# Optimization experiments

Measured on AMD Instinct MI355X. Metric: run time of the kernel, lower is better.

Reference implementation:

```python
import jax, jax.numpy as jnp
import numpy as np

EMBED_DIM = 1024
NUM_HEADS = 16
HEAD_DIM = EMBED_DIM // NUM_HEADS
SCALE = HEAD_DIM ** -0.5


def setup_inputs() -> dict:
    key = jax.random.key(0)
    ks = jax.random.split(key, 5)
    B, N, C = 4, 2048, EMBED_DIM
    s = C ** -0.5
    return {
        "x": jax.random.normal(ks[0], (B, N, C), dtype=jnp.float32),
        "w_qkv": jax.random.normal(ks[1], (C, 3 * C), dtype=jnp.float32) * s,
        "b_qkv": jnp.zeros((3 * C,), dtype=jnp.float32),
        "w_proj": jax.random.normal(ks[2], (C, C), dtype=jnp.float32) * s,
        "b_proj": jnp.zeros((C,), dtype=jnp.float32),
    }


def reference(x, w_qkv, b_qkv, w_proj, b_proj):
    B, N, C = x.shape
    H, D = NUM_HEADS, HEAD_DIM
    qkv = x @ w_qkv + b_qkv                      # (B, N, 3C)
    qkv = qkv.reshape(B, N, 3, H, D)
    qkv = jnp.transpose(qkv, (2, 0, 3, 1, 4))    # (3, B, H, N, D)
    q, k, v = qkv[0], qkv[1], qkv[2]
    attn = jnp.einsum('bhnd,bhmd->bhnm', q, k) * SCALE
    attn = jax.nn.softmax(attn, axis=-1)
    out = jnp.einsum('bhnm,bhmd->bhnd', attn, v)  # (B, H, N, D)
    out = jnp.transpose(out, (0, 2, 1, 3)).reshape(B, N, C)
    return out @ w_proj + b_proj
```

## Files before the change

kernel.cpp:

```cpp
#include <hip/hip_runtime.h>

typedef __attribute__((ext_vector_type(8))) short short8v;
typedef __attribute__((ext_vector_type(4))) short short4v;
typedef __attribute__((ext_vector_type(4))) float float4v;
typedef __attribute__((ext_vector_type(4))) unsigned short ushort4v;
typedef __attribute__((ext_vector_type(8))) unsigned short ushort8v;

#define GLOBAL_AS __attribute__((address_space(1)))
#define LDS_AS __attribute__((address_space(3)))

__device__ __forceinline__ void async_cp16(const void* g, void* l) {
  __builtin_amdgcn_global_load_lds((const GLOBAL_AS void*)g, (LDS_AS void*)l, 16, 0, 0);
}

__device__ __forceinline__ unsigned short f2bf(float f) {
  unsigned u = __float_as_uint(f);
  u += 0x7fffu + ((u >> 16) & 1u);
  return (unsigned short)(u >> 16);
}

#if defined(__HIP_DEVICE_COMPILE__)
#if __has_builtin(__builtin_amdgcn_exp2f)
#define EXP2F(x) __builtin_amdgcn_exp2f(x)
#else
#define EXP2F(x) exp2f(x)
#endif
#else
#define EXP2F(x) exp2f(x)
#endif

#if defined(__HIP_DEVICE_COMPILE__) && __has_builtin(__builtin_amdgcn_cvt_pk_bf16_f32)
typedef __attribute__((ext_vector_type(2))) __bf16 bf16x2v;
__device__ __forceinline__ unsigned pk_bf16(float a, float b) {
  bf16x2v r = __builtin_amdgcn_cvt_pk_bf16_f32(a, b);
  return __builtin_bit_cast(unsigned, r);
}
#else
__device__ __forceinline__ unsigned pk_bf16(float a, float b) {
  return (unsigned)f2bf(a) | ((unsigned)f2bf(b) << 16);
}
#endif

#define MFMA_QK(a, b, c) __builtin_amdgcn_mfma_f32_16x16x32_bf16(a, b, c, 0, 0, 0)

__device__ __forceinline__ void wg_barrier() {
  asm volatile("" ::: "memory");
  __builtin_amdgcn_s_barrier();
  asm volatile("" ::: "memory");
}


__global__ __launch_bounds__(256) void cvt_f32_bf16(const float* __restrict__ src,
                                                    unsigned short* __restrict__ dst) {
  int i = blockIdx.x * 256 + threadIdx.x;
  float4 v = ((const float4*)src)[i];
  ushort4v o;
  o.x = f2bf(v.x); o.y = f2bf(v.y); o.z = f2bf(v.z); o.w = f2bf(v.w);
  ((ushort4v*)dst)[i] = o;
}

__global__ __launch_bounds__(256) void transpose_w(const float* __restrict__ src,
                                                   unsigned short* __restrict__ dst,
                                                   int K, int N) {
  __shared__ float tile[64][65];
  int k0 = blockIdx.x * 64, n0 = blockIdx.y * 64;
  int t = threadIdx.x;
  int tc = t & 15, tr = t >> 4;
#pragma unroll
  for (int p = 0; p < 4; p++) {
    int r = tr + p * 16;
    float4 v = *(const float4*)(src + (size_t)(k0 + r) * N + n0 + tc * 4);
    tile[r][tc * 4 + 0] = v.x; tile[r][tc * 4 + 1] = v.y;
    tile[r][tc * 4 + 2] = v.z; tile[r][tc * 4 + 3] = v.w;
  }
  __syncthreads();
#pragma unroll
  for (int p = 0; p < 4; p++) {
    int rn = tr + p * 16;
    ushort4v o;
    o.x = f2bf(tile[tc * 4 + 0][rn]);
    o.y = f2bf(tile[tc * 4 + 1][rn]);
    o.z = f2bf(tile[tc * 4 + 2][rn]);
    o.w = f2bf(tile[tc * 4 + 3][rn]);
    *(ushort4v*)(dst + (size_t)(n0 + rn) * K + k0 + tc * 4) = o;
  }
}

__device__ __forceinline__ void stage128x32(const unsigned short* __restrict__ src,
                                            unsigned short* dst, int r0, int k0, int tid) {
#pragma unroll
  for (int p = 0; p < 2; p++) {
    int idx = p * 256 + tid;
    int row = idx >> 2, s = idx & 3;
    int ch = s ^ ((row >> 1) & 3);
    async_cp16(src + (size_t)(r0 + row) * 1024 + k0 + ch * 8, dst + idx * 8);
  }
}


#define TT_STRIDE 136

__global__ __launch_bounds__(256) void gemm_qkv(const unsigned short* __restrict__ A,
                                                const unsigned short* __restrict__ BT,
                                                const float* __restrict__ bias,
                                                unsigned short* __restrict__ Qo,
                                                unsigned short* __restrict__ Ko,
                                                unsigned short* __restrict__ VTo) {
  __shared__ unsigned short smem[24576];
  int tid = threadIdx.x;
  int lane = tid & 63, w = tid >> 6, g = lane >> 4, c = lane & 15;
  int m0 = blockIdx.x * 128, n0 = blockIdx.y * 128;
  int wm = (w & 1) * 64, wn = (w >> 1) * 64;
  float4v acc[4][4] = {};

  stage128x32(A, smem + 0 * 4096, m0, 0, tid);
  stage128x32(BT, smem + 12288 + 0 * 4096, n0, 0, tid);
  stage128x32(A, smem + 1 * 4096, m0, 32, tid);
  stage128x32(BT, smem + 12288 + 1 * 4096, n0, 32, tid);
  asm volatile("s_waitcnt vmcnt(4)" ::: "memory");
  wg_barrier();

  int cb = 0;
  for (int t = 0; t < 32; ++t) {
    int nb = cb + 2; if (nb >= 3) nb -= 3;
    const unsigned short* Ap = smem + cb * 4096;
    const unsigned short* Bp = smem + 12288 + cb * 4096;

    short8v af[4], bf[4];
#pragma unroll
    for (int i = 0; i < 4; i++) {
      int r = wm + i * 16 + c;
      af[i] = *(const short8v*)(Ap + r * 32 + (g ^ ((r >> 1) & 3)) * 8);
    }
#pragma unroll
    for (int j = 0; j < 4; j++) {
      int r = wn + j * 16 + c;
      bf[j] = *(const short8v*)(Bp + r * 32 + (g ^ ((r >> 1) & 3)) * 8);
    }

    if (t + 2 < 32) {
      stage128x32(A, smem + nb * 4096, m0, (t + 2) * 32, tid);
      stage128x32(BT, smem + 12288 + nb * 4096, n0, (t + 2) * 32, tid);
    }

    __builtin_amdgcn_s_setprio(1);
#pragma unroll
    for (int i = 0; i < 4; i++)
#pragma unroll
      for (int j = 0; j < 4; j++)
        acc[i][j] = MFMA_QK(af[i], bf[j], acc[i][j]);
    __builtin_amdgcn_s_setprio(0);

    if (t < 30) { asm volatile("s_waitcnt vmcnt(4)" ::: "memory"); }
    else        { asm volatile("s_waitcnt vmcnt(0)" ::: "memory"); }
    wg_barrier();
    cb = cb + 1 == 3 ? 0 : cb + 1;
  }

  int which = n0 >> 10;
  if (which != 2) {
#pragma unroll
    for (int j = 0; j < 4; j++) {
      int ng = n0 + wn + j * 16 + c;
      float bv = bias[ng];
      int h = (ng & 1023) >> 6, d = ng & 63;
#pragma unroll
      for (int i = 0; i < 4; i++) {
#pragma unroll
        for (int r = 0; r < 4; r++) {
          int mg = m0 + wm + i * 16 + g * 4 + r;
          int b = mg >> 11, n = mg & 2047;
          float v = acc[i][j][r] + bv;
          if (which == 0)
            Qo[((size_t)(b * 16 + h) * 2048 + n) * 64 + d] = f2bf(v * 0.18033688011112042f);
          else
            Ko[((size_t)(b * 16 + h) * 2048 + n) * 64 + d] = f2bf(v);
        }
      }
    }
  } else {
    __syncthreads();
#pragma unroll
    for (int j = 0; j < 4; j++) {
      int nl = wn + j * 16 + c;
      float bv = bias[n0 + nl];
#pragma unroll
      for (int i = 0; i < 4; i++) {
        int ml = wm + i * 16 + g * 4;
        unsigned p0 = pk_bf16(acc[i][j][0] + bv, acc[i][j][1] + bv);
        unsigned p1 = pk_bf16(acc[i][j][2] + bv, acc[i][j][3] + bv);
        *(unsigned*)(smem + nl * TT_STRIDE + ml) = p0;
        *(unsigned*)(smem + nl * TT_STRIDE + ml + 2) = p1;
      }
    }
    __syncthreads();
    int rr = lane >> 4, tc = lane & 15;
    int P = tc & 3, g32 = tc >> 2;
    int b = m0 >> 11, mloc = m0 & 2047;
    int h0 = (n0 & 1023) >> 6;
#pragma unroll
    for (int s = 0; s < 8; s++) {
      int row = w * 32 + s * 4 + rr;
      int h = h0 + (row >> 6), d = row & 63;
      const unsigned short* bp = smem + row * TT_STRIDE + g32 * 32 + P * 4;
      union { unsigned long long q[2]; ushort8v v; } u;
      u.q[0] = *(const unsigned long long*)(bp);
      u.q[1] = *(const unsigned long long*)(bp + 16);
      size_t gaddr = ((size_t)(b * 16 + h) * 64 + d) * 2048 + mloc + g32 * 32 + P * 8;
      *(ushort8v*)(VTo + gaddr) = u.v;
    }
  }
}


#define NTOK 2048
#define BK 64

__device__ __forceinline__ short8v exppack(float4v a, float4v b2) {
  a.x = EXP2F(a.x); a.y = EXP2F(a.y); a.z = EXP2F(a.z); a.w = EXP2F(a.w);
  b2.x = EXP2F(b2.x); b2.y = EXP2F(b2.y); b2.z = EXP2F(b2.z); b2.w = EXP2F(b2.w);
  union { unsigned u[4]; short8v s; } cv;
  cv.u[0] = pk_bf16(a.x, a.y);
  cv.u[1] = pk_bf16(a.z, a.w);
  cv.u[2] = pk_bf16(b2.x, b2.y);
  cv.u[3] = pk_bf16(b2.z, b2.w);
  return cv.s;
}

__global__ __launch_bounds__(256, 2) void attn_kernel(const unsigned short* __restrict__ Qg,
                                                      const unsigned short* __restrict__ Kg,
                                                      const unsigned short* __restrict__ VTg,
                                                      unsigned short* __restrict__ Og) {
  __shared__ unsigned short Ks[2][BK * 64];
  __shared__ unsigned short VTs[2][64 * BK];

  int tid = threadIdx.x;
  int lane = tid & 63, w = tid >> 6, g = lane >> 4, c = lane & 15;
  int id = blockIdx.x;
  int xcd = id & 7, within = id >> 3;
  int bh = xcd * 8 + (within >> 3);
  int q0 = (within & 7) * 256;

  const unsigned short* Qb = Qg + (size_t)bh * NTOK * 64;
  const unsigned short* Kb = Kg + (size_t)bh * NTOK * 64;
  const unsigned short* VTb = VTg + (size_t)bh * 64 * NTOK;

  short8v qf[4][2];
#pragma unroll
  for (int nt = 0; nt < 4; nt++)
#pragma unroll
    for (int kk = 0; kk < 2; kk++)
      qf[nt][kk] = *(const short8v*)(Qb + (size_t)(q0 + w * 64 + nt * 16 + c) * 64 +
                                     kk * 32 + g * 8);

  short8v ones8;
#pragma unroll
  for (int i = 0; i < 8; i++) ones8[i] = (short)0x3F80;

  float4v lacc[4] = {};
  float4v o[4][4] = {};

#pragma unroll
  for (int p = 0; p < 2; p++) {
    int idx = p * 256 + tid;
    int row = idx >> 3, ch = idx & 7;
    async_cp16(Kb + (size_t)row * 64 + ((ch ^ (row & 7)) * 8), &Ks[0][idx * 8]);
    async_cp16(VTb + (size_t)row * NTOK + ((ch ^ (row & 7)) * 8), &VTs[0][idx * 8]);
  }

  for (int it = 0; it < NTOK / BK; it++) {
    int pb = it & 1;
    __syncthreads();

    if (it + 1 < NTOK / BK) {
      int kt = (it + 1) * BK;
#pragma unroll
      for (int p = 0; p < 2; p++) {
        int idx = p * 256 + tid;
        int row = idx >> 3, ch = idx & 7;
        async_cp16(Kb + (size_t)(kt + row) * 64 + ((ch ^ (row & 7)) * 8),
                   &Ks[1 - pb][idx * 8]);
        async_cp16(VTb + (size_t)row * NTOK + kt + ((ch ^ (row & 7)) * 8),
                   &VTs[1 - pb][idx * 8]);
      }
    }

    const unsigned short* Kp = &Ks[pb][0];
    const unsigned short* Vp = &VTs[pb][0];

    float4v stA[2][4] = {};
    float4v stB[2][4] = {};

    __builtin_amdgcn_s_setprio(1);
#pragma unroll
    for (int mth = 0; mth < 2; mth++) {
      int row = mth * 16 + c;
      short8v kf[2];
#pragma unroll
      for (int kk = 0; kk < 2; kk++) {
        int ch = (kk * 4 + g) ^ (row & 7);
        kf[kk] = *(const short8v*)(Kp + row * 64 + ch * 8);
      }
#pragma unroll
      for (int nt = 0; nt < 4; nt++)
#pragma unroll
        for (int kk = 0; kk < 2; kk++)
          stA[mth][nt] = MFMA_QK(kf[kk], qf[nt][kk], stA[mth][nt]);
    }
#pragma unroll
    for (int mth = 0; mth < 2; mth++) {
      int row = (2 + mth) * 16 + c;
      short8v kf[2];
#pragma unroll
      for (int kk = 0; kk < 2; kk++) {
        int ch = (kk * 4 + g) ^ (row & 7);
        kf[kk] = *(const short8v*)(Kp + row * 64 + ch * 8);
      }
#pragma unroll
      for (int nt = 0; nt < 4; nt++)
#pragma unroll
        for (int kk = 0; kk < 2; kk++)
          stB[mth][nt] = MFMA_QK(kf[kk], qf[nt][kk], stB[mth][nt]);
    }
    __builtin_amdgcn_s_setprio(0);

    short8v pa8A[4];
#pragma unroll
    for (int nt = 0; nt < 4; nt++) pa8A[nt] = exppack(stA[0][nt], stA[1][nt]);

    __builtin_amdgcn_s_setprio(1);
#pragma unroll
    for (int nt_o = 0; nt_o < 4; nt_o++) {
      int d = nt_o * 16 + c;
      int s = g ^ (d & 7);
      short8v vb8 = *(const short8v*)(Vp + d * BK + s * 8);
#pragma unroll
      for (int mt = 0; mt < 4; mt++)
        o[mt][nt_o] = MFMA_QK(pa8A[mt], vb8, o[mt][nt_o]);
    }
#pragma unroll
    for (int mt = 0; mt < 4; mt++)
      lacc[mt] = MFMA_QK(pa8A[mt], ones8, lacc[mt]);
    __builtin_amdgcn_s_setprio(0);

    short8v pa8B[4];
#pragma unroll
    for (int nt = 0; nt < 4; nt++) pa8B[nt] = exppack(stB[0][nt], stB[1][nt]);

    __builtin_amdgcn_s_setprio(1);
#pragma unroll
    for (int nt_o = 0; nt_o < 4; nt_o++) {
      int d = nt_o * 16 + c;
      int s = (4 + g) ^ (d & 7);
      short8v vb8 = *(const short8v*)(Vp + d * BK + s * 8);
#pragma unroll
      for (int mt = 0; mt < 4; mt++)
        o[mt][nt_o] = MFMA_QK(pa8B[mt], vb8, o[mt][nt_o]);
    }
#pragma unroll
    for (int mt = 0; mt < 4; mt++)
      lacc[mt] = MFMA_QK(pa8B[mt], ones8, lacc[mt]);
    __builtin_amdgcn_s_setprio(0);
  }

  int b = bh >> 4, h = bh & 15;
#pragma unroll
  for (int mt = 0; mt < 4; mt++) {
    float4v li;
#pragma unroll
    for (int r = 0; r < 4; r++) li[r] = 1.0f / lacc[mt][r];
#pragma unroll
    for (int nt_o = 0; nt_o < 4; nt_o++) {
      float4v v = o[mt][nt_o] * li;
      int col = h * 64 + nt_o * 16 + c;
      int rowbase = b * NTOK + q0 + w * 64 + mt * 16 + g * 4;
#pragma unroll
      for (int r = 0; r < 4; r++)
        Og[(size_t)(rowbase + r) * 1024 + col] = f2bf(v[r]);
    }
  }
}

__global__ __launch_bounds__(256) void gemm_proj(const unsigned short* __restrict__ A,
                                                 const unsigned short* __restrict__ BT,
                                                 const float* __restrict__ bias,
                                                 float* __restrict__ out) {
  __shared__ unsigned short smem[24576];
  int tid = threadIdx.x;
  int lane = tid & 63, w = tid >> 6, g = lane >> 4, c = lane & 15;
  int m0 = blockIdx.x * 128, n0 = blockIdx.y * 128;
  int wm = (w & 1) * 64, wn = (w >> 1) * 64;
  float4v acc[4][4] = {};

  stage128x32(A, smem + 0 * 4096, m0, 0, tid);
  stage128x32(BT, smem + 12288 + 0 * 4096, n0, 0, tid);
  stage128x32(A, smem + 1 * 4096, m0, 32, tid);
  stage128x32(BT, smem + 12288 + 1 * 4096, n0, 32, tid);
  asm volatile("s_waitcnt vmcnt(4)" ::: "memory");
  wg_barrier();

  int cb = 0;
  for (int t = 0; t < 32; ++t) {
    int nb = cb + 2; if (nb >= 3) nb -= 3;
    const unsigned short* Ap = smem + cb * 4096;
    const unsigned short* Bp = smem + 12288 + cb * 4096;

    short8v af[4], bf[4];
#pragma unroll
    for (int i = 0; i < 4; i++) {
      int r = wm + i * 16 + c;
      af[i] = *(const short8v*)(Ap + r * 32 + (g ^ ((r >> 1) & 3)) * 8);
    }
#pragma unroll
    for (int j = 0; j < 4; j++) {
      int r = wn + j * 16 + c;
      bf[j] = *(const short8v*)(Bp + r * 32 + (g ^ ((r >> 1) & 3)) * 8);
    }

    if (t + 2 < 32) {
      stage128x32(A, smem + nb * 4096, m0, (t + 2) * 32, tid);
      stage128x32(BT, smem + 12288 + nb * 4096, n0, (t + 2) * 32, tid);
    }

    __builtin_amdgcn_s_setprio(1);
#pragma unroll
    for (int i = 0; i < 4; i++)
#pragma unroll
      for (int j = 0; j < 4; j++)
        acc[i][j] = MFMA_QK(af[i], bf[j], acc[i][j]);
    __builtin_amdgcn_s_setprio(0);

    if (t < 30) { asm volatile("s_waitcnt vmcnt(4)" ::: "memory"); }
    else        { asm volatile("s_waitcnt vmcnt(0)" ::: "memory"); }
    wg_barrier();
    cb = cb + 1 == 3 ? 0 : cb + 1;
  }

#pragma unroll
  for (int j = 0; j < 4; j++) {
    int ng = n0 + wn + j * 16 + c;
    float bv = bias[ng];
#pragma unroll
    for (int i = 0; i < 4; i++) {
#pragma unroll
      for (int r = 0; r < 4; r++) {
        int mg = m0 + wm + i * 16 + g * 4 + r;
        out[(size_t)mg * 1024 + ng] = acc[i][j][r] + bv;
      }
    }
  }
}


extern "C" void kernel_launch(void* const* d_in, const int* in_sizes, int n_in,
                              void* d_out, int out_size, void* d_ws, size_t ws_size,
                              hipStream_t stream) {
  (void)in_sizes; (void)n_in; (void)out_size; (void)ws_size;
  const float* x = (const float*)d_in[0];
  const float* w_qkv = (const float*)d_in[1];
  const float* b_qkv = (const float*)d_in[2];
  const float* w_proj = (const float*)d_in[3];
  const float* b_proj = (const float*)d_in[4];
  float* out = (float*)d_out;

  unsigned short* x_bf = (unsigned short*)d_ws;
  unsigned short* wqkvT = x_bf + (size_t)8192 * 1024;
  unsigned short* wprojT = wqkvT + (size_t)3072 * 1024;
  unsigned short* qws = wprojT + (size_t)1024 * 1024;
  unsigned short* kws = qws + (size_t)8388608;
  unsigned short* vtws = kws + (size_t)8388608;
  unsigned short* aws = vtws + (size_t)8388608;

  cvt_f32_bf16<<<8192, 256, 0, stream>>>(x, x_bf);
  transpose_w<<<dim3(16, 48), 256, 0, stream>>>(w_qkv, wqkvT, 1024, 3072);
  transpose_w<<<dim3(16, 16), 256, 0, stream>>>(w_proj, wprojT, 1024, 1024);
  gemm_qkv<<<dim3(64, 24), 256, 0, stream>>>(x_bf, wqkvT, b_qkv, qws, kws, vtws);
  attn_kernel<<<512, 256, 0, stream>>>(qws, kws, vtws, aws);
  gemm_proj<<<dim3(64, 8), 256, 0, stream>>>(aws, wprojT, b_proj, out);
}
```

Measured before the change: 265.9 us.

## Halve attention query tile and load V directly from global

The attention kernel now processes 128 queries per block (32 per wave) instead of 256, doubling the grid to 1024 blocks and raising launch bounds to 4 blocks per CU. The V^T tile is no longer staged in LDS through async copies. Each lane reads its V fragments straight from global memory, which halves LDS use and cuts the registers needed for accumulators. The aim is higher occupancy and better latency hiding. In exchange, K tiles are reused across fewer queries, K/V traffic rises, and direct global V loads may stall the MFMA chain.

```diff
diff --git a/kernel.cpp b/kernel.cpp
--- a/kernel.cpp
+++ b/kernel.cpp
@@ -227,45 +227,45 @@
   return cv.s;
 }
 
-__global__ __launch_bounds__(256, 2) void attn_kernel(const unsigned short* __restrict__ Qg,
+__global__ __launch_bounds__(256, 4) void attn_kernel(const unsigned short* __restrict__ Qg,
                                                       const unsigned short* __restrict__ Kg,
                                                       const unsigned short* __restrict__ VTg,
                                                       unsigned short* __restrict__ Og) {
   __shared__ unsigned short Ks[2][BK * 64];
-  __shared__ unsigned short VTs[2][64 * BK];
 
   int tid = threadIdx.x;
   int lane = tid & 63, w = tid >> 6, g = lane >> 4, c = lane & 15;
   int id = blockIdx.x;
   int xcd = id & 7, within = id >> 3;
-  int bh = xcd * 8 + (within >> 3);
-  int q0 = (within & 7) * 256;
+  int bh = xcd * 8 + (within >> 4);
+  int q0 = (within & 15) * 128;
 
   const unsigned short* Qb = Qg + (size_t)bh * NTOK * 64;
   const unsigned short* Kb = Kg + (size_t)bh * NTOK * 64;
   const unsigned short* VTb = VTg + (size_t)bh * 64 * NTOK;
 
-  short8v qf[4][2];
-#pragma unroll
-  for (int nt = 0; nt < 4; nt++)
+  short8v qf[2][2];
+#pragma unroll
+  for (int nt = 0; nt < 2; nt++)
 #pragma unroll
     for (int kk = 0; kk < 2; kk++)
-      qf[nt][kk] = *(const short8v*)(Qb + (size_t)(q0 + w * 64 + nt * 16 + c) * 64 +
+      qf[nt][kk] = *(const short8v*)(Qb + (size_t)(q0 + w * 32 + nt * 16 + c) * 64 +
                                      kk * 32 + g * 8);
 
   short8v ones8;
 #pragma unroll
   for (int i = 0; i < 8; i++) ones8[i] = (short)0x3F80;
 
-  float4v lacc[4] = {};
-  float4v o[4][4] = {};
+  float4v lacc[2] = {};
+  float4v o[2][4] = {};
+
+  const unsigned short* vbase = VTb + (size_t)c * 2048 + g * 8;
 
 #pragma unroll
   for (int p = 0; p < 2; p++) {
     int idx = p * 256 + tid;
     int row = idx >> 3, ch = idx & 7;
     async_cp16(Kb + (size_t)row * 64 + ((ch ^ (row & 7)) * 8), &Ks[0][idx * 8]);
-    async_cp16(VTb + (size_t)row * NTOK + ((ch ^ (row & 7)) * 8), &VTs[0][idx * 8]);
   }
 
   for (int it = 0; it < NTOK / BK; it++) {
@@ -280,92 +280,58 @@
         int row = idx >> 3, ch = idx & 7;
         async_cp16(Kb + (size_t)(kt + row) * 64 + ((ch ^ (row & 7)) * 8),
                    &Ks[1 - pb][idx * 8]);
-        async_cp16(VTb + (size_t)row * NTOK + kt + ((ch ^ (row & 7)) * 8),
-                   &VTs[1 - pb][idx * 8]);
       }
     }
 
     const unsigned short* Kp = &Ks[pb][0];
-    const unsigned short* Vp = &VTs[pb][0];
-
-    float4v stA[2][4] = {};
-    float4v stB[2][4] = {};
-
-    __builtin_amdgcn_s_setprio(1);
-#pragma unroll
-    for (int mth = 0; mth < 2; mth++) {
-      int row = mth * 16 + c;
-      short8v kf[2];
-#pragma unroll
-      for (int kk = 0; kk < 2; kk++) {
-        int ch = (kk * 4 + g) ^ (row & 7);
-        kf[kk] = *(const short8v*)(Kp + row * 64 + ch * 8);
+
+#pragma unroll
+    for (int t = 0; t < 2; t++) {
+      int ch32 = it * 2 + t;
+      short8v vb[4];
+#pragma unroll
+      for (int nt_o = 0; nt_o < 4; nt_o++)
+        vb[nt_o] = *(const short8v*)(vbase + (size_t)nt_o * 32768 + ch32 * 32);
+
+      float4v st[2][2] = {};
+      __builtin_amdgcn_s_setprio(1);
+#pragma unroll
+      for (int mth = 0; mth < 2; mth++) {
+        int row = (t * 2 + mth) * 16 + c;
+        short8v kf[2];
+#pragma unroll
+        for (int kk = 0; kk < 2; kk++) {
+          int ch = (kk * 4 + g) ^ (row & 7);
+          kf[kk] = *(const short8v*)(Kp + row * 64 + ch * 8);
+        }
+#pragma unroll
+        for (int nt = 0; nt < 2; nt++)
+#pragma unroll
+          for (int kk = 0; kk < 2; kk++)
+            st[mth][nt] = MFMA_QK(kf[kk], qf[nt][kk], st[mth][nt]);
       }
-#pragma unroll
-      for (int nt = 0; nt < 4; nt++)
-#pragma unroll
-        for (int kk = 0; kk < 2; kk++)
-          stA[mth][nt] = MFMA_QK(kf[kk], qf[nt][kk], stA[mth][nt]);
-    }
-#pragma unroll
-    for (int mth = 0; mth < 2; mth++) {
-      int row = (2 + mth) * 16 + c;
-      short8v kf[2];
-#pragma unroll
-      for (int kk = 0; kk < 2; kk++) {
-        int ch = (kk * 4 + g) ^ (row & 7);
-        kf[kk] = *(const short8v*)(Kp + row * 64 + ch * 8);
-      }
-#pragma unroll
-      for (int nt = 0; nt < 4; nt++)
-#pragma unroll
-        for (int kk = 0; kk < 2; kk++)
-          stB[mth][nt] = MFMA_QK(kf[kk], qf[nt][kk], stB[mth][nt]);
-    }
-    __builtin_amdgcn_s_setprio(0);
-
-    short8v pa8A[4];
-#pragma unroll
-    for (int nt = 0; nt < 4; nt++) pa8A[nt] = exppack(stA[0][nt], stA[1][nt]);
-
-    __builtin_amdgcn_s_setprio(1);
-#pragma unroll
-    for (int nt_o = 0; nt_o < 4; nt_o++) {
-      int d = nt_o * 16 + c;
-      int s = g ^ (d & 7);
-      short8v vb8 = *(const short8v*)(Vp + d * BK + s * 8);
-#pragma unroll
-      for (int mt = 0; mt < 4; mt++)
-        o[mt][nt_o] = MFMA_QK(pa8A[mt], vb8, o[mt][nt_o]);
-    }
-#pragma unroll
-    for (int mt = 0; mt < 4; mt++)
-      lacc[mt] = MFMA_QK(pa8A[mt], ones8, lacc[mt]);
-    __builtin_amdgcn_s_setprio(0);
-
-    short8v pa8B[4];
-#pragma unroll
-    for (int nt = 0; nt < 4; nt++) pa8B[nt] = exppack(stB[0][nt], stB[1][nt]);
-
-    __builtin_amdgcn_s_setprio(1);
-#pragma unroll
-    for (int nt_o = 0; nt_o < 4; nt_o++) {
-      int d = nt_o * 16 + c;
-      int s = (4 + g) ^ (d & 7);
-      short8v vb8 = *(const short8v*)(Vp + d * BK + s * 8);
-#pragma unroll
-      for (int mt = 0; mt < 4; mt++)
-        o[mt][nt_o] = MFMA_QK(pa8B[mt], vb8, o[mt][nt_o]);
-    }
-#pragma unroll
-    for (int mt = 0; mt < 4; mt++)
-      lacc[mt] = MFMA_QK(pa8B[mt], ones8, lacc[mt]);
-    __builtin_amdgcn_s_setprio(0);
+      __builtin_amdgcn_s_setprio(0);
+
+      short8v pa8[2];
+#pragma unroll
+      for (int nt = 0; nt < 2; nt++) pa8[nt] = exppack(st[0][nt], st[1][nt]);
+
+      __builtin_amdgcn_s_setprio(1);
+#pragma unroll
+      for (int nt_o = 0; nt_o < 4; nt_o++)
+#pragma unroll
+        for (int mt = 0; mt < 2; mt++)
+          o[mt][nt_o] = MFMA_QK(pa8[mt], vb[nt_o], o[mt][nt_o]);
+#pragma unroll
+      for (int mt = 0; mt < 2; mt++)
+        lacc[mt] = MFMA_QK(pa8[mt], ones8, lacc[mt]);
+      __builtin_amdgcn_s_setprio(0);
+    }
   }
 
   int b = bh >> 4, h = bh & 15;
 #pragma unroll
-  for (int mt = 0; mt < 4; mt++) {
+  for (int mt = 0; mt < 2; mt++) {
     float4v li;
 #pragma unroll
     for (int r = 0; r < 4; r++) li[r] = 1.0f / lacc[mt][r];
@@ -373,7 +339,7 @@
     for (int nt_o = 0; nt_o < 4; nt_o++) {
       float4v v = o[mt][nt_o] * li;
       int col = h * 64 + nt_o * 16 + c;
-      int rowbase = b * NTOK + q0 + w * 64 + mt * 16 + g * 4;
+      int rowbase = b * NTOK + q0 + w * 32 + mt * 16 + g * 4;
 #pragma unroll
       for (int r = 0; r < 4; r++)
         Og[(size_t)(rowbase + r) * 1024 + col] = f2bf(v[r]);
@@ -475,6 +441,6 @@
   transpose_w<<<dim3(16, 48), 256, 0, stream>>>(w_qkv, wqkvT, 1024, 3072);
   transpose_w<<<dim3(16, 16), 256, 0, stream>>>(w_proj, wprojT, 1024, 1024);
   gemm_qkv<<<dim3(64, 24), 256, 0, stream>>>(x_bf, wqkvT, b_qkv, qws, kws, vtws);
-  attn_kernel<<<512, 256, 0, stream>>>(qws, kws, vtws, aws);
+  attn_kernel<<<1024, 256, 0, stream>>>(qws, kws, vtws, aws);
   gemm_proj<<<dim3(64, 8), 256, 0, stream>>>(aws, wprojT, b_proj, out);
 }
```

Measured after the change: 311.7 us. 1.17x slower.
